# Optimization experiments

Measured on AMD Instinct MI355X. Metric: run time of the kernel, lower is better.

## Reference

```python
import jax, jax.numpy as jnp
import numpy as np

EMBED = 64
HEADS = 8
N, S = 8, 1024


def setup_inputs() -> dict:
    key = jax.random.key(0)
    ks = jax.random.split(key, 8)
    scale = 1.0 / np.sqrt(EMBED)
    return {
        "values": jax.random.normal(ks[0], (N, S, EMBED), dtype=jnp.float32),
        "keys": jax.random.normal(ks[1], (N, S, EMBED), dtype=jnp.float32),
        "queries": jax.random.normal(ks[2], (N, S, EMBED), dtype=jnp.float32),
        # per-head projection weights, torch Linear convention: y = x @ W.T
        "Wv": jax.random.normal(ks[3], (HEADS, EMBED, EMBED), dtype=jnp.float32) * scale,
        "Wk": jax.random.normal(ks[4], (HEADS, EMBED, EMBED), dtype=jnp.float32) * scale,
        "Wq": jax.random.normal(ks[5], (HEADS, EMBED, EMBED), dtype=jnp.float32) * scale,
        "Wout": jax.random.normal(ks[6], (EMBED, HEADS * EMBED), dtype=jnp.float32) * (1.0 / np.sqrt(HEADS * EMBED)),
        "bout": jnp.zeros((EMBED,), dtype=jnp.float32),
    }


def reference(values, keys, queries, Wv, Wk, Wq, Wout, bout):
    d = queries.shape[-1]
    # Batched per-head projections (each head keeps full embed dim, per the module)
    v = jnp.einsum("nkd,hed->nhke", values, Wv)   # [N,H,K,D]
    k = jnp.einsum("nkd,hed->nhke", keys, Wk)     # [N,H,K,D]
    q = jnp.einsum("nqd,hed->nhqe", queries, Wq)  # [N,H,Q,D]
    energy = jnp.einsum("nhqd,nhkd->nhqk", q, k)
    attn = jax.nn.softmax(energy / jnp.sqrt(jnp.asarray(d, energy.dtype)), axis=-1)  # [N,H,Q,K]
    head_out = jnp.einsum("nhqk,nhkd->nhqd", attn, v)  # [N,H,Q,D]
    # torch.cat(output_heads, dim=2) == transpose heads next to feature then flatten
    nN, nH, nQ, nD = head_out.shape
    cat = jnp.transpose(head_out, (0, 2, 1, 3)).reshape(nN, nQ, nH * nD)  # [N,Q,H*D]
    out = cat @ Wout.T + bout  # [N,Q,D]
    return out, attn
```

## Files before the change

### kernel.cpp

```cpp
#include <hip/hip_runtime.h>

typedef __bf16 bf16x8 __attribute__((ext_vector_type(8)));
typedef __bf16 bf16x4 __attribute__((ext_vector_type(4)));
typedef float  f32x4  __attribute__((ext_vector_type(4)));

#define MFMA16(a, b, c) __builtin_amdgcn_mfma_f32_16x16x32_bf16((a), (b), (c), 0, 0, 0)

constexpr int N_ = 8, H_ = 8, S_ = 1024, D_ = 64;

__global__ __launch_bounds__(256) void proj_kernel(
    const float* __restrict__ Xq, const float* __restrict__ Xk,
    const float* __restrict__ Xv,
    const float* __restrict__ Wq, const float* __restrict__ Wk,
    const float* __restrict__ Wv,
    unsigned short* __restrict__ qb_, unsigned short* __restrict__ kb_,
    unsigned short* __restrict__ vtb_)
{
    __shared__ __bf16 T[64 * 72];

    const int which = blockIdx.y;
    const float* X = (which == 0) ? Xq : (which == 1) ? Xk : Xv;
    const float* W = (which == 0) ? Wq : (which == 1) ? Wk : Wv;

    const int b   = blockIdx.x;
    const int st  = b & 15;
    const int h   = (b >> 4) & 7;
    const int n   = b >> 7;
    const int s0  = st * 64;
    const int nh  = n * H_ + h;
    const int tid = threadIdx.x;
    const int w = tid >> 6, lane = tid & 63;
    const int l16 = lane & 15, quad = lane >> 4;

    const float* xrow = X + (size_t)(n * S_ + s0 + w * 16 + l16) * D_;
    bf16x8 a[2];
#pragma unroll
    for (int half = 0; half < 2; ++half) {
        const float* p = xrow + half * 32 + quad * 8;
        f32x4 x0 = *(const f32x4*)p;
        f32x4 x1 = *(const f32x4*)(p + 4);
#pragma unroll
        for (int j = 0; j < 4; ++j) { a[half][j] = (__bf16)x0[j]; a[half][4 + j] = (__bf16)x1[j]; }
    }

#pragma unroll
    for (int et = 0; et < 4; ++et) {
        const int e0 = et * 16;
        f32x4 acc = {0.f, 0.f, 0.f, 0.f};
#pragma unroll
        for (int half = 0; half < 2; ++half) {
            const float* wp = W + ((size_t)(h * 64 + e0 + l16)) * 64 + half * 32 + quad * 8;
            f32x4 x0 = *(const f32x4*)wp;
            f32x4 x1 = *(const f32x4*)(wp + 4);
            bf16x8 bf;
#pragma unroll
            for (int j = 0; j < 4; ++j) { bf[j] = (__bf16)x0[j]; bf[4 + j] = (__bf16)x1[j]; }
            acc = MFMA16(a[half], bf, acc);
        }
#pragma unroll
        for (int r = 0; r < 4; ++r) {
            const int sl = w * 16 + quad * 4 + r;
            const int e  = e0 + l16;
            const __bf16 v = (__bf16)acc[r];
            if (which == 2) T[e * 72 + sl] = v;
            else            T[sl * 72 + e] = v;
        }
    }
    __syncthreads();

    const int row = tid >> 2, seg = tid & 3;
    const bf16x8 d0 = *(const bf16x8*)&T[row * 72 + seg * 16];
    const bf16x8 d1 = *(const bf16x8*)&T[row * 72 + seg * 16 + 8];
    __bf16* dst;
    if (which == 2)
        dst = (__bf16*)vtb_ + ((size_t)nh * 64 + row) * S_ + s0 + seg * 16;
    else
        dst = (__bf16*)(which == 0 ? qb_ : kb_) + ((size_t)nh * S_ + s0 + row) * D_ + seg * 16;
    *(bf16x8*)dst = d0;
    *(bf16x8*)(dst + 8) = d1;
}

__global__ __launch_bounds__(256, 4) void attn_kernel(
    const unsigned short* __restrict__ qb_, const unsigned short* __restrict__ kb_,
    const unsigned short* __restrict__ vtb_,
    float* __restrict__ attn_out, unsigned short* __restrict__ catb_)
{
    const __bf16* qb  = (const __bf16*)qb_;
    const __bf16* kb  = (const __bf16*)kb_;
    const __bf16* vtb = (const __bf16*)vtb_;
    __bf16* catb = (__bf16*)catb_;

    const int b  = blockIdx.x;
    const int qt = b & 15;
    const int h  = (b >> 4) & 7;
    const int n  = b >> 7;
    const int nh = n * H_ + h;
    const int q0 = qt * 64;

    const int tid = threadIdx.x;
    const int w = tid >> 6, lane = tid & 63;
    const int l16 = lane & 15, quad = lane >> 4;
    const int m0 = w * 16;

    const __bf16* qbase = qb + ((size_t)(nh * S_ + q0 + m0 + l16)) * D_;
    const bf16x8 aq0 = *(const bf16x8*)(qbase + quad * 8);
    const bf16x8 aq1 = *(const bf16x8*)(qbase + 32 + quad * 8);

    const __bf16* kbase = kb + ((size_t)(nh * S_ + l16)) * D_ + quad * 8;

    float ssum = 0.f;
#pragma unroll 4
    for (int kt = 0; kt < 64; ++kt) {
        const __bf16* kp = kbase + (size_t)kt * 16 * D_;
        const bf16x8 b0 = *(const bf16x8*)kp;
        const bf16x8 b1 = *(const bf16x8*)(kp + 32);
        f32x4 c = {0.f, 0.f, 0.f, 0.f};
        c = MFMA16(b0, aq0, c);
        c = MFMA16(b1, aq1, c);
#pragma unroll
        for (int r = 0; r < 4; ++r) ssum += __expf(c[r] * 0.125f);
    }
    ssum += __shfl_xor(ssum, 16);
    ssum += __shfl_xor(ssum, 32);
    const float inv = 1.0f / ssum;

    float* abase = attn_out + ((size_t)(nh * S_ + q0 + m0 + l16)) * S_;
    const __bf16* vbase = vtb + ((size_t)(nh * 64 + l16)) * S_ + quad * 8;

    const int lo_addr = (((quad & 1) * 2) * 16 + l16) * 4;
    const int hi_addr = lo_addr + 64;
    const bool hiq = (quad & 2) != 0;

    f32x4 acc[4] = {{0.f,0.f,0.f,0.f},{0.f,0.f,0.f,0.f},{0.f,0.f,0.f,0.f},{0.f,0.f,0.f,0.f}};

#pragma unroll 2
    for (int ch = 0; ch < 32; ++ch) {
        unsigned Wt[2][2];
#pragma unroll
        for (int t = 0; t < 2; ++t) {
            const int kt = ch * 2 + t;
            const __bf16* kp = kbase + (size_t)kt * 16 * D_;
            const bf16x8 b0 = *(const bf16x8*)kp;
            const bf16x8 b1 = *(const bf16x8*)(kp + 32);
            f32x4 c = {0.f, 0.f, 0.f, 0.f};
            c = MFMA16(b0, aq0, c);
            c = MFMA16(b1, aq1, c);
            float p[4];
#pragma unroll
            for (int r = 0; r < 4; ++r) p[r] = __expf(c[r] * 0.125f) * inv;
#pragma unroll
            for (int pr = 0; pr < 2; ++pr) {
                const __bf16 ha = (__bf16)p[2 * pr], hb = (__bf16)p[2 * pr + 1];
                const unsigned ua = *(const unsigned short*)&ha;
                const unsigned ub = *(const unsigned short*)&hb;
                Wt[t][pr] = ua | (ub << 16);
            }
        }
        const int s00 = __builtin_amdgcn_ds_bpermute(lo_addr, (int)Wt[0][0]);
        const int s10 = __builtin_amdgcn_ds_bpermute(lo_addr, (int)Wt[1][0]);
        const int s01 = __builtin_amdgcn_ds_bpermute(lo_addr, (int)Wt[0][1]);
        const int s11 = __builtin_amdgcn_ds_bpermute(lo_addr, (int)Wt[1][1]);
        const int s02 = __builtin_amdgcn_ds_bpermute(hi_addr, (int)Wt[0][0]);
        const int s12 = __builtin_amdgcn_ds_bpermute(hi_addr, (int)Wt[1][0]);
        const int s03 = __builtin_amdgcn_ds_bpermute(hi_addr, (int)Wt[0][1]);
        const int s13 = __builtin_amdgcn_ds_bpermute(hi_addr, (int)Wt[1][1]);
        union { bf16x8 v; unsigned u[4]; } pf;
        pf.u[0] = (unsigned)(hiq ? s10 : s00);
        pf.u[1] = (unsigned)(hiq ? s11 : s01);
        pf.u[2] = (unsigned)(hiq ? s12 : s02);
        pf.u[3] = (unsigned)(hiq ? s13 : s03);

#pragma unroll
        for (int et = 0; et < 4; ++et) {
            const bf16x8 bv = *(const bf16x8*)(vbase + (size_t)et * 16 * S_ + ch * 32);
            acc[et] = MFMA16(pf.v, bv, acc[et]);
        }

        f32x4 f0, f1;
#pragma unroll
        for (int j = 0; j < 4; ++j) { f0[j] = (float)pf.v[j]; f1[j] = (float)pf.v[4 + j]; }
        float* ap = abase + ch * 32 + quad * 8;
        *(f32x4*)ap = f0;
        *(f32x4*)(ap + 4) = f1;
    }

#pragma unroll
    for (int r = 0; r < 4; ++r) {
        const int s = q0 + m0 + quad * 4 + r;
        __bf16* cp = catb + ((size_t)n * S_ + s) * (H_ * D_) + h * D_ + l16;
#pragma unroll
        for (int et = 0; et < 4; ++et) cp[et * 16] = (__bf16)acc[et][r];
    }
}

__global__ __launch_bounds__(256) void outproj_kernel(
    const unsigned short* __restrict__ catb_, const float* __restrict__ Wout,
    const float* __restrict__ bout, float* __restrict__ out)
{
    __shared__ float R[4 * 16 * 68];

    const __bf16* catb = (const __bf16*)catb_;
    const int r0  = blockIdx.x * 16;
    const int tid = threadIdx.x;
    const int w = tid >> 6, lane = tid & 63;
    const int l16 = lane & 15, quad = lane >> 4;
    const int k0 = w * 128;

    const __bf16* arow  = catb + (size_t)(r0 + l16) * 512 + k0 + quad * 8;
    const float*  wbase = Wout + (size_t)l16 * 512 + k0 + quad * 8;

    f32x4 acc[4] = {{0.f,0.f,0.f,0.f},{0.f,0.f,0.f,0.f},{0.f,0.f,0.f,0.f},{0.f,0.f,0.f,0.f}};

#pragma unroll
    for (int kc = 0; kc < 4; ++kc) {
        const bf16x8 af = *(const bf16x8*)(arow + kc * 32);
#pragma unroll
        for (int et = 0; et < 4; ++et) {
            const float* wp = wbase + (size_t)et * 16 * 512 + kc * 32;
            f32x4 x0 = *(const f32x4*)wp;
            f32x4 x1 = *(const f32x4*)(wp + 4);
            bf16x8 bf;
#pragma unroll
            for (int j = 0; j < 4; ++j) { bf[j] = (__bf16)x0[j]; bf[4 + j] = (__bf16)x1[j]; }
            acc[et] = MFMA16(af, bf, acc[et]);
        }
    }
#pragma unroll
    for (int et = 0; et < 4; ++et)
#pragma unroll
        for (int r = 0; r < 4; ++r)
            R[w * (16 * 68) + (quad * 4 + r) * 68 + et * 16 + l16] = acc[et][r];
    __syncthreads();

    const int row = tid >> 4, c0 = (tid & 15) * 4;
    f32x4 s = *(const f32x4*)&R[row * 68 + c0];
#pragma unroll
    for (int wv = 1; wv < 4; ++wv) s += *(const f32x4*)&R[wv * (16 * 68) + row * 68 + c0];
    s += *(const f32x4*)(bout + c0);
    *(f32x4*)(out + (size_t)(r0 + row) * 64 + c0) = s;
}

extern "C" void kernel_launch(void* const* d_in, const int* in_sizes, int n_in,
                              void* d_out, int out_size, void* d_ws, size_t ws_size,
                              hipStream_t stream)
{
    const float* values  = (const float*)d_in[0];
    const float* keys    = (const float*)d_in[1];
    const float* queries = (const float*)d_in[2];
    const float* Wv      = (const float*)d_in[3];
    const float* Wk      = (const float*)d_in[4];
    const float* Wq      = (const float*)d_in[5];
    const float* Wout    = (const float*)d_in[6];
    const float* bout    = (const float*)d_in[7];

    float* out  = (float*)d_out;
    float* attn = out + (size_t)N_ * S_ * D_;

    const size_t nelem = (size_t)N_ * H_ * S_ * D_;
    unsigned short* qb   = (unsigned short*)d_ws;
    unsigned short* kb   = qb  + nelem;
    unsigned short* vtb  = kb  + nelem;
    unsigned short* catb = vtb + nelem;

    proj_kernel<<<dim3(N_ * H_ * (S_ / 64), 3), 256, 0, stream>>>(
        queries, keys, values, Wq, Wk, Wv, qb, kb, vtb);
    attn_kernel<<<N_ * H_ * (S_ / 64), 256, 0, stream>>>(qb, kb, vtb, attn, catb);
    outproj_kernel<<<(N_ * S_) / 16, 256, 0, stream>>>(catb, Wout, bout, out);
}
```

Before: 478.4 us.

## Split attention key range across wave pairs with LDS reduction and smaller query tiles

The attention kernel now handles 32 query rows per block instead of 64. The four waves split into two row groups times two key halves. Softmax row sums and the partial PV accumulators are combined through shared memory with barriers. The grid doubles and a block-index swizzle spreads heads across XCDs, and launch bounds ask for 8 blocks per CU. The aim is more parallelism and better latency hiding for a kernel dominated by the attention-matrix stores, at the cost of extra syncs, LDS use and some register pressure.

```diff
diff --git a/kernel.cpp b/kernel.cpp
--- a/kernel.cpp
+++ b/kernel.cpp
@@ -80,37 +80,43 @@
     *(bf16x8*)(dst + 8) = d1;
 }
 
-__global__ __launch_bounds__(256, 4) void attn_kernel(
+__global__ __launch_bounds__(256, 8) void attn_kernel(
     const unsigned short* __restrict__ qb_, const unsigned short* __restrict__ kb_,
     const unsigned short* __restrict__ vtb_,
     float* __restrict__ attn_out, unsigned short* __restrict__ catb_)
 {
+    __shared__ float Sred[4 * 16];
+    __shared__ float Ored[2 * 16 * 68];
+
     const __bf16* qb  = (const __bf16*)qb_;
     const __bf16* kb  = (const __bf16*)kb_;
     const __bf16* vtb = (const __bf16*)vtb_;
     __bf16* catb = (__bf16*)catb_;
 
-    const int b  = blockIdx.x;
-    const int qt = b & 15;
-    const int h  = (b >> 4) & 7;
-    const int n  = b >> 7;
-    const int nh = n * H_ + h;
-    const int q0 = qt * 64;
+    const int bid = blockIdx.x;
+    const int b   = (bid & 7) * 256 + (bid >> 3);
+    const int qt  = b & 31;
+    const int h   = (b >> 5) & 7;
+    const int n   = b >> 8;
+    const int nh  = n * H_ + h;
+    const int q0  = qt * 32;
 
     const int tid = threadIdx.x;
     const int w = tid >> 6, lane = tid & 63;
     const int l16 = lane & 15, quad = lane >> 4;
-    const int m0 = w * 16;
-
-    const __bf16* qbase = qb + ((size_t)(nh * S_ + q0 + m0 + l16)) * D_;
+    const int rw = w & 1;
+    const int kw = w >> 1;
+    const int k0 = kw * 512;
+
+    const __bf16* qbase = qb + ((size_t)(nh * S_ + q0 + rw * 16 + l16)) * D_;
     const bf16x8 aq0 = *(const bf16x8*)(qbase + quad * 8);
     const bf16x8 aq1 = *(const bf16x8*)(qbase + 32 + quad * 8);
 
-    const __bf16* kbase = kb + ((size_t)(nh * S_ + l16)) * D_ + quad * 8;
+    const __bf16* kbase = kb + ((size_t)(nh * S_ + k0 + l16)) * D_ + quad * 8;
 
     float ssum = 0.f;
 #pragma unroll 4
-    for (int kt = 0; kt < 64; ++kt) {
+    for (int kt = 0; kt < 32; ++kt) {
         const __bf16* kp = kbase + (size_t)kt * 16 * D_;
         const bf16x8 b0 = *(const bf16x8*)kp;
         const bf16x8 b1 = *(const bf16x8*)(kp + 32);
@@ -122,10 +128,12 @@
     }
     ssum += __shfl_xor(ssum, 16);
     ssum += __shfl_xor(ssum, 32);
-    const float inv = 1.0f / ssum;
-
-    float* abase = attn_out + ((size_t)(nh * S_ + q0 + m0 + l16)) * S_;
-    const __bf16* vbase = vtb + ((size_t)(nh * 64 + l16)) * S_ + quad * 8;
+    if (lane < 16) Sred[w * 16 + lane] = ssum;
+    __syncthreads();
+    const float inv = 1.0f / (Sred[w * 16 + l16] + Sred[(w ^ 2) * 16 + l16]);
+
+    float* abase = attn_out + ((size_t)(nh * S_ + q0 + rw * 16 + l16)) * S_ + k0;
+    const __bf16* vbase = vtb + ((size_t)(nh * 64 + l16)) * S_ + k0 + quad * 8;
 
     const int lo_addr = (((quad & 1) * 2) * 16 + l16) * 4;
     const int hi_addr = lo_addr + 64;
@@ -134,7 +142,7 @@
     f32x4 acc[4] = {{0.f,0.f,0.f,0.f},{0.f,0.f,0.f,0.f},{0.f,0.f,0.f,0.f},{0.f,0.f,0.f,0.f}};
 
 #pragma unroll 2
-    for (int ch = 0; ch < 32; ++ch) {
+    for (int ch = 0; ch < 16; ++ch) {
         unsigned Wt[2][2];
 #pragma unroll
         for (int t = 0; t < 2; ++t) {
@@ -184,12 +192,27 @@
         *(f32x4*)(ap + 4) = f1;
     }
 
-#pragma unroll
-    for (int r = 0; r < 4; ++r) {
-        const int s = q0 + m0 + quad * 4 + r;
-        __bf16* cp = catb + ((size_t)n * S_ + s) * (H_ * D_) + h * D_ + l16;
-#pragma unroll
-        for (int et = 0; et < 4; ++et) cp[et * 16] = (__bf16)acc[et][r];
+    __syncthreads();
+    if (kw == 1) {
+#pragma unroll
+        for (int et = 0; et < 4; ++et)
+#pragma unroll
+            for (int r = 0; r < 4; ++r)
+                Ored[rw * (16 * 68) + (quad * 4 + r) * 68 + et * 16 + l16] = acc[et][r];
+    }
+    __syncthreads();
+    if (kw == 0) {
+#pragma unroll
+        for (int r = 0; r < 4; ++r) {
+            const int s = q0 + rw * 16 + quad * 4 + r;
+            __bf16* cp = catb + ((size_t)n * S_ + s) * (H_ * D_) + h * D_ + l16;
+#pragma unroll
+            for (int et = 0; et < 4; ++et) {
+                const float o = acc[et][r] +
+                    Ored[rw * (16 * 68) + (quad * 4 + r) * 68 + et * 16 + l16];
+                cp[et * 16] = (__bf16)o;
+            }
+        }
     }
 }
 
@@ -264,6 +287,6 @@
 
     proj_kernel<<<dim3(N_ * H_ * (S_ / 64), 3), 256, 0, stream>>>(
         queries, keys, values, Wq, Wk, Wv, qb, kb, vtb);
-    attn_kernel<<<N_ * H_ * (S_ / 64), 256, 0, stream>>>(qb, kb, vtb, attn, catb);
+    attn_kernel<<<N_ * H_ * (S_ / 32), 256, 0, stream>>>(qb, kb, vtb, attn, catb);
     outproj_kernel<<<(N_ * S_) / 16, 256, 0, stream>>>(catb, Wout, bout, out);
 }
```

After: 482.7 us. Within noise of the previous version (+0.9%).
